# Performance work log

Measured on AMD Instinct MI355X. Metric: run time of the kernel, lower is better.

The kernel has to match this reference:

```python
import jax, jax.numpy as jnp
import numpy as np

B, H, WD, C = 16, 96, 96, 256
WS, SH, NH = 6, 3, 8
N = WS * WS
ALPHA = (2 * 6) ** 0.25  # deepnorm alpha, n_layers=6
SCALE = (C // NH) ** 0.5  # faithful to source: head_dim**0.5 (not **-0.5)
EPS = 1e-5


def _rel_index(ws):
    coords = np.stack(np.meshgrid(np.arange(ws), np.arange(ws), indexing='ij'))  # (2,ws,ws)
    flat = coords.reshape(2, -1)
    rel = (flat[:, :, None] - flat[:, None, :]).transpose(1, 2, 0).copy()
    rel[..., 0] += ws - 1
    rel[..., 1] += ws - 1
    rel[..., 0] *= 2 * ws - 1
    return jnp.asarray(rel.sum(-1))  # (N,N) int


def _attn_mask(h, w, ws, sh):
    img = np.zeros((h, w))
    cnt = 0
    for hs in (slice(0, -ws), slice(-ws, -sh), slice(-sh, None)):
        for wsl in (slice(0, -ws), slice(-ws, -sh), slice(-sh, None)):
            img[hs, wsl] = cnt
            cnt += 1
    win = img.reshape(h // ws, ws, w // ws, ws).transpose(0, 2, 1, 3).reshape(-1, ws * ws)
    diff = win[:, None, :] - win[:, :, None]
    return jnp.asarray(np.where(diff != 0, -100.0, 0.0), jnp.float32)  # (nW,N,N)


def _ln(t, w, b):
    mu = jnp.mean(t, -1, keepdims=True)
    var = jnp.var(t, -1, keepdims=True)
    return (t - mu) * jax.lax.rsqrt(var + EPS) * w + b


def setup_inputs() -> dict:
    key = jax.random.key(0)
    ks = jax.random.split(key, 8)
    d = {
        'x': jax.random.normal(ks[0], (B, H * WD, C), jnp.float32),
        'qkv_w': jax.random.normal(ks[1], (C, 3 * C), jnp.float32) * 0.02,
        'qkv_b': jnp.zeros((3 * C,), jnp.float32),
        'bias_table': jax.random.normal(ks[2], ((2 * WS - 1) ** 2, NH), jnp.float32) * 0.02,
        'proj_w': jax.random.normal(ks[3], (C, C), jnp.float32) * 0.02,
        'proj_b': jnp.zeros((C,), jnp.float32),
        'norm1_w': jnp.ones((C,), jnp.float32),
        'norm1_b': jnp.zeros((C,), jnp.float32),
        'norm2_w': jnp.ones((C,), jnp.float32),
        'norm2_b': jnp.zeros((C,), jnp.float32),
        'fc1_w': jax.random.normal(ks[4], (C, 4 * C), jnp.float32) * 0.02,
        'fc1_b': jnp.zeros((4 * C,), jnp.float32),
        'fc2_w': jax.random.normal(ks[5], (4 * C, C), jnp.float32) * 0.02,
        'fc2_b': jnp.zeros((C,), jnp.float32),
    }
    return d


def reference(x, qkv_w, qkv_b, bias_table, proj_w, proj_b, norm1_w, norm1_b,
              norm2_w, norm2_b, fc1_w, fc1_b, fc2_w, fc2_b):
    hd = C // NH
    nW = (H // WS) * (WD // WS)
    shortcut = x  # (B, L, C), norm_before=False -> post-norm
    xs = x.reshape(B, H, WD, C)
    xs = jnp.roll(xs, (-SH, -SH), axis=(1, 2))  # cyclic shift
    # window partition -> (B*nW, N, C)
    xw = xs.reshape(B, H // WS, WS, WD // WS, WS, C).transpose(0, 1, 3, 2, 4, 5).reshape(B * nW, N, C)
    qkv = (xw @ qkv_w + qkv_b).reshape(B * nW, N, 3, NH, hd).transpose(2, 0, 3, 1, 4)
    q, k, v = qkv[0] * SCALE, qkv[1], qkv[2]
    attn = jnp.einsum('bhnd,bhmd->bhnm', q, k)  # (B*nW, H, N, N)
    bias = bias_table[_rel_index(WS).reshape(-1)].reshape(N, N, NH).transpose(2, 0, 1)
    attn = attn + bias[None]
    mask = _attn_mask(H, WD, WS, SH)  # (nW, N, N)
    attn = attn.reshape(B, nW, NH, N, N) + mask[None, :, None]
    attn = jax.nn.softmax(attn.reshape(B * nW, NH, N, N), axis=-1)
    out = jnp.einsum('bhnm,bhmd->bhnd', attn, v).transpose(0, 2, 1, 3).reshape(B * nW, N, C)
    out = out @ proj_w + proj_b
    # faithful buggy window_reverse: identity permute == plain reshape
    xs = out.reshape(B, H // WS, WS, WD // WS, WS, C).reshape(B, H, WD, C)
    xs = jnp.roll(xs, (SH, SH), axis=(1, 2))
    x1 = _ln(shortcut * ALPHA + xs.reshape(B, H * WD, C), norm1_w, norm1_b)
    hmid = jax.nn.gelu(x1 @ fc1_w + fc1_b, approximate=False)
    x2 = _ln(x1 * ALPHA + (hmid @ fc2_w + fc2_b), norm2_w, norm2_b)
    return x2
```

## Files before the change

kernel.cpp:

```cpp
#include <hip/hip_runtime.h>
#include <math.h>

typedef __bf16 bf16x8 __attribute__((ext_vector_type(8)));
typedef __bf16 bf16x4 __attribute__((ext_vector_type(4)));
typedef short  s16x4  __attribute__((ext_vector_type(4)));
typedef float  f32x4  __attribute__((ext_vector_type(4)));

#define NTOK 147456
#define LTOK 9216
#define ALPHA 1.8612097182041991f
#define QSCALE 5.656854249492380196f
#define MFMA32(a,b,c) __builtin_amdgcn_mfma_f32_16x16x32_bf16((a),(b),(c),0,0,0)
#define SWB(row,kb) ((kb) ^ ((row)&7))

__device__ __forceinline__ f32x4 MFMA16(bf16x4 a, bf16x4 b, f32x4 c) {
#if __has_builtin(__builtin_amdgcn_mfma_f32_16x16x16bf16_1k)
    return __builtin_amdgcn_mfma_f32_16x16x16bf16_1k(*(s16x4*)&a, *(s16x4*)&b, c, 0, 0, 0);
#else
    f32x4 d = c;
    asm volatile("s_nop 1\n\ts_nop 1\n\t"
                 "v_mfma_f32_16x16x16_bf16 %0, %1, %2, %0\n\t"
                 "s_nop 7\n\ts_nop 7"
                 : "+v"(d) : "v"(a), "v"(b));
    return d;
#endif
}

__device__ __forceinline__ float gelu_sig(float x) {
    const float e = __expf(-1.702f * x);
    return x * __builtin_amdgcn_rcpf(1.0f + e);
}

__device__ __forceinline__ void gll16(const void* g, void* l) {
    __builtin_amdgcn_global_load_lds(
        (const __attribute__((address_space(1))) void*)g,
        (__attribute__((address_space(3))) void*)l, 16, 0, 0);
}

__global__ __launch_bounds__(256) void k0_prep(
    const float* __restrict__ qkv_w, const float* __restrict__ proj_w,
    const float* __restrict__ fc1_w, const float* __restrict__ fc2_w,
    __bf16* __restrict__ qkvT, __bf16* __restrict__ projT,
    __bf16* __restrict__ w1T, __bf16* __restrict__ w2T)
{
    const int id = blockIdx.x * 256 + threadIdx.x;
    if (id < 196608) {
        const int o = id >> 8, k = id & 255;
        qkvT[id] = (__bf16)qkv_w[k * 768 + o];
    } else if (id < 262144) {
        const int i = id - 196608, o = i >> 8, k = i & 255;
        projT[i] = (__bf16)proj_w[k * 256 + o];
    } else if (id < 524288) {
        const int i = id - 262144, o = i >> 8, k = i & 255;
        w1T[i] = (__bf16)fc1_w[k * 1024 + o];
    } else {
        const int i = id - 524288, o = i >> 10, k = i & 1023;
        w2T[i] = (__bf16)fc2_w[k * 256 + o];
    }
}

__global__ __launch_bounds__(512, 4) void k1f_qkv_attn(
    const float* __restrict__ x, const __bf16* __restrict__ qkvT,
    const float* __restrict__ qkv_b, const float* __restrict__ bias_table,
    __bf16* __restrict__ attnout)
{
    __shared__ __attribute__((aligned(16))) char SM[77824];
    typedef __bf16 (*a256_t)[256];
    typedef __bf16 (*b32_t)[32];
    a256_t As = (a256_t)SM;
    b32_t  Bs = (b32_t)(SM + 24576);
    int*   srcrow = (int*)(SM + 73728);
    float* bias_s = (float*)(SM + 73920);

    const int t = threadIdx.x;
    const int wid = t >> 6, lane = t & 63;
    const int l15 = lane & 15, lg = lane >> 4;
    const int blk = blockIdx.x;
    const int win = blk & 255;
    const int wh = win >> 4, ww = win & 15;
    const int h = wid;

    if (t < 48) {
        int n = t; if (n > 35) n = 35;
        const int b = blk >> 8;
        const int gh = (wh * 6 + n / 6 + 3) % 96;
        const int gw = (ww * 6 + n % 6 + 3) % 96;
        srcrow[t] = b * LTOK + gh * 96 + gw;
    }
    for (int o = t; o < 968; o += 512) bias_s[o] = bias_table[o];
    __syncthreads();

    for (int o = t; o < 48 * 32; o += 512) {
        const int row = o >> 5, kb = o & 31;
        const float* src = x + (size_t)srcrow[row] * 256 + kb * 8;
        const float4 f0 = *(const float4*)src;
        const float4 f1 = *(const float4*)(src + 4);
        bf16x8 p;
        p[0] = (__bf16)f0.x; p[1] = (__bf16)f0.y; p[2] = (__bf16)f0.z; p[3] = (__bf16)f0.w;
        p[4] = (__bf16)f1.x; p[5] = (__bf16)f1.y; p[6] = (__bf16)f1.z; p[7] = (__bf16)f1.w;
        *(bf16x8*)&As[row][SWB(row, kb) * 8] = p;
    }

    const f32x4 fzero = {0.f, 0.f, 0.f, 0.f};
    f32x4 accQ[2][3], accK[2][3], accV[2][3];
    #pragma unroll
    for (int c = 0; c < 2; ++c)
        #pragma unroll
        for (int r = 0; r < 3; ++r) { accQ[c][r] = fzero; accK[c][r] = fzero; accV[c][r] = fzero; }

    for (int kc = 0; kc < 8; ++kc) {
        __syncthreads();
        #pragma unroll
        for (int i = 0; i < 6; ++i) {
            const int r0 = wid * 96 + i * 16;
            const int row = r0 + (lane >> 2), kbl = lane & 3;
            gll16(qkvT + (size_t)row * 256 + kc * 32 + ((kbl ^ (row & 3)) * 8),
                  &Bs[r0][0]);
        }
        __syncthreads();
        bf16x8 af[3];
        #pragma unroll
        for (int rt = 0; rt < 3; ++rt) {
            const int ar = rt * 16 + l15;
            const int kb = kc * 4 + lg;
            af[rt] = *(const bf16x8*)&As[ar][SWB(ar, kb) * 8];
        }
        #pragma unroll
        for (int ct = 0; ct < 2; ++ct) {
            const int brq = h * 32 + ct * 16 + l15;
            const bf16x8 bq = *(const bf16x8*)&Bs[brq][((lg ^ (brq & 3))) * 8];
            const int brk = 256 + brq;
            const bf16x8 bk = *(const bf16x8*)&Bs[brk][((lg ^ (brk & 3))) * 8];
            const int brv = 512 + brq;
            const bf16x8 bv = *(const bf16x8*)&Bs[brv][((lg ^ (brv & 3))) * 8];
            #pragma unroll
            for (int rt = 0; rt < 3; ++rt) {
                accQ[ct][rt] = MFMA32(bq, af[rt], accQ[ct][rt]);
                accK[ct][rt] = MFMA32(bk, af[rt], accK[ct][rt]);
                accV[ct][rt] = MFMA32(af[rt], bv, accV[ct][rt]);
            }
        }
    }

    bf16x4 qf[3][2], kf[3][2], vf[2][3];
    #pragma unroll
    for (int dh = 0; dh < 2; ++dh) {
        #pragma unroll
        for (int q = 0; q < 4; ++q) {
            const float qb = qkv_b[h * 32 + dh * 16 + lg * 4 + q];
            const float kb = qkv_b[256 + h * 32 + dh * 16 + lg * 4 + q];
            #pragma unroll
            for (int rt = 0; rt < 3; ++rt) {
                qf[rt][dh][q] = (__bf16)((accQ[dh][rt][q] + qb) * QSCALE);
                kf[rt][dh][q] = (__bf16)(accK[dh][rt][q] + kb);
            }
        }
    }
    #pragma unroll
    for (int cd = 0; cd < 2; ++cd) {
        const float vb = qkv_b[512 + h * 32 + cd * 16 + l15];
        #pragma unroll
        for (int c3 = 0; c3 < 3; ++c3)
            #pragma unroll
            for (int q = 0; q < 4; ++q)
                vf[cd][c3][q] = (__bf16)(accV[cd][c3][q] + vb);
    }

    f32x4 s[3][3];
    #pragma unroll
    for (int qt = 0; qt < 3; ++qt)
        #pragma unroll
        for (int c3 = 0; c3 < 3; ++c3) {
            f32x4 acc = MFMA16(kf[c3][0], qf[qt][0], fzero);
            s[qt][c3] = MFMA16(kf[c3][1], qf[qt][1], acc);
        }

    int i2_[3][4], j2_[3][4], g2_[3][4];
    #pragma unroll
    for (int c3 = 0; c3 < 3; ++c3)
        #pragma unroll
        for (int q = 0; q < 4; ++q) {
            const int kt = c3 * 16 + lg * 4 + q;
            const int kk2 = kt < 36 ? kt : 35;
            i2_[c3][q] = kk2 / 6; j2_[c3][q] = kk2 - i2_[c3][q] * 6;
            g2_[c3][q] = ((wh < 15) ? 0 : (i2_[c3][q] < 3 ? 1 : 2)) * 3
                       + ((ww < 15) ? 0 : (j2_[c3][q] < 3 ? 1 : 2));
        }

    bf16x4 pa[3][3];
    #pragma unroll
    for (int qt = 0; qt < 3; ++qt) {
        const int qtok = qt * 16 + l15;
        const int nn = qtok < 36 ? qtok : 35;
        const int i1 = nn / 6, j1 = nn - i1 * 6;
        const int g1 = ((wh < 15) ? 0 : (i1 < 3 ? 1 : 2)) * 3
                     + ((ww < 15) ? 0 : (j1 < 3 ? 1 : 2));
        float vals[3][4];
        float mx = -1e30f;
        #pragma unroll
        for (int c3 = 0; c3 < 3; ++c3)
            #pragma unroll
            for (int q = 0; q < 4; ++q) {
                const int kt = c3 * 16 + lg * 4 + q;
                float v;
                if (kt < 36) {
                    v = s[qt][c3][q]
                      + bias_s[((i1 - i2_[c3][q] + 5) * 11 + (j1 - j2_[c3][q] + 5)) * 8 + h];
                    if (g1 != g2_[c3][q]) v -= 100.0f;
                } else {
                    v = -1e30f;
                }
                vals[c3][q] = v;
                mx = fmaxf(mx, v);
            }
        mx = fmaxf(mx, __shfl_xor(mx, 16));
        mx = fmaxf(mx, __shfl_xor(mx, 32));
        float sum = 0.f;
        #pragma unroll
        for (int c3 = 0; c3 < 3; ++c3)
            #pragma unroll
            for (int q = 0; q < 4; ++q) {
                const float e = __expf(vals[c3][q] - mx);
                vals[c3][q] = e;
                sum += e;
            }
        sum += __shfl_xor(sum, 16);
        sum += __shfl_xor(sum, 32);
        const float inv = 1.0f / sum;
        #pragma unroll
        for (int c3 = 0; c3 < 3; ++c3)
            #pragma unroll
            for (int q = 0; q < 4; ++q)
                pa[qt][c3][q] = (__bf16)(vals[c3][q] * inv);
    }

    const size_t rowbase = (size_t)blk * 36;
    #pragma unroll
    for (int qt = 0; qt < 3; ++qt)
        #pragma unroll
        for (int cd = 0; cd < 2; ++cd) {
            f32x4 o = MFMA16(pa[qt][0], vf[cd][0], fzero);
            o = MFMA16(pa[qt][1], vf[cd][1], o);
            o = MFMA16(pa[qt][2], vf[cd][2], o);
            #pragma unroll
            for (int q = 0; q < 4; ++q) {
                const int n = qt * 16 + lg * 4 + q;
                if (n < 36)
                    attnout[(rowbase + n) * 256 + h * 32 + cd * 16 + l15] = (__bf16)o[q];
            }
        }
}

__global__ __launch_bounds__(512) void k2_proj_ln(
    const __bf16* __restrict__ attnout, const __bf16* __restrict__ projT,
    const float* __restrict__ proj_b, const float* __restrict__ x,
    const float* __restrict__ n1w, const float* __restrict__ n1b,
    __bf16* __restrict__ x1b)
{
    __shared__ __attribute__((aligned(16))) __bf16 As[128][64];
    __shared__ __attribute__((aligned(16))) __bf16 Bs[256][64];
    __shared__ float ps[128][4], ps2[128][4];
    const int t = threadIdx.x;
    const int wid = t >> 6, lane = t & 63;
    const int l15 = lane & 15, lg = lane >> 4;
    const int mb = blockIdx.x;
    const int wm = wid >> 2, wn = wid & 3;

    const f32x4 fzero = {0.f, 0.f, 0.f, 0.f};
    f32x4 acc[4][4];
    #pragma unroll
    for (int i = 0; i < 4; ++i)
        #pragma unroll
        for (int j = 0; j < 4; ++j) acc[i][j] = fzero;

    for (int kc = 0; kc < 4; ++kc) {
        __syncthreads();
        #pragma unroll
        for (int i = 0; i < 2; ++i) {
            const int r0 = wid * 16 + i * 8;
            const int row = r0 + (lane >> 3), kbl = lane & 7;
            gll16(attnout + (size_t)(mb * 128 + row) * 256 + kc * 64 + ((kbl ^ (row & 7)) * 8),
                  &As[r0][0]);
        }
        #pragma unroll
        for (int i = 0; i < 4; ++i) {
            const int r0 = wid * 32 + i * 8;
            const int row = r0 + (lane >> 3), kbl = lane & 7;
            gll16(projT + (size_t)row * 256 + kc * 64 + ((kbl ^ (row & 7)) * 8),
                  &Bs[r0][0]);
        }
        __syncthreads();
        #pragma unroll
        for (int kk = 0; kk < 2; ++kk) {
            bf16x8 af[4], bfr[4];
            #pragma unroll
            for (int rt = 0; rt < 4; ++rt) {
                const int ar = wm * 64 + rt * 16 + l15;
                af[rt] = *(const bf16x8*)&As[ar][((kk * 4 + lg) ^ (ar & 7)) * 8];
            }
            #pragma unroll
            for (int ct = 0; ct < 4; ++ct) {
                const int br = wn * 64 + ct * 16 + l15;
                bfr[ct] = *(const bf16x8*)&Bs[br][((kk * 4 + lg) ^ (br & 7)) * 8];
            }
            #pragma unroll
            for (int rt = 0; rt < 4; ++rt)
                #pragma unroll
                for (int ct = 0; ct < 4; ++ct)
                    acc[rt][ct] = MFMA32(af[rt], bfr[ct], acc[rt][ct]);
        }
    }

    int dtok_[4][4];
    #pragma unroll
    for (int rt = 0; rt < 4; ++rt) {
        #pragma unroll
        for (int q = 0; q < 4; ++q) {
            const int rowl = wm * 64 + rt * 16 + lg * 4 + q;
            const int tok = mb * 128 + rowl;
            const int b = tok / LTOK, l = tok % LTOK;
            const int hh = l / 96, wwp = l % 96;
            const int dtok = b * LTOK + ((hh + 3) % 96) * 96 + ((wwp + 3) % 96);
            dtok_[rt][q] = dtok;
            float s = 0.f, s2 = 0.f;
            #pragma unroll
            for (int ct = 0; ct < 4; ++ct) {
                const int col = wn * 64 + ct * 16 + l15;
                const float v = acc[rt][ct][q] + proj_b[col] + ALPHA * x[(size_t)dtok * 256 + col];
                acc[rt][ct][q] = v;
                s += v; s2 += v * v;
            }
            s  += __shfl_xor(s, 1, 16);  s += __shfl_xor(s, 2, 16);
            s  += __shfl_xor(s, 4, 16);  s += __shfl_xor(s, 8, 16);
            s2 += __shfl_xor(s2, 1, 16); s2 += __shfl_xor(s2, 2, 16);
            s2 += __shfl_xor(s2, 4, 16); s2 += __shfl_xor(s2, 8, 16);
            if (l15 == 0) { ps[rowl][wn] = s; ps2[rowl][wn] = s2; }
        }
    }
    __syncthreads();
    #pragma unroll
    for (int rt = 0; rt < 4; ++rt) {
        #pragma unroll
        for (int q = 0; q < 4; ++q) {
            const int rowl = wm * 64 + rt * 16 + lg * 4 + q;
            const float S  = ps[rowl][0] + ps[rowl][1] + ps[rowl][2] + ps[rowl][3];
            const float S2 = ps2[rowl][0] + ps2[rowl][1] + ps2[rowl][2] + ps2[rowl][3];
            const float mu = S * (1.0f / 256.0f);
            const float var = S2 * (1.0f / 256.0f) - mu * mu;
            const float rstd = rsqrtf(var + 1e-5f);
            __bf16* op = x1b + (size_t)dtok_[rt][q] * 256;
            #pragma unroll
            for (int ct = 0; ct < 4; ++ct) {
                const int col = wn * 64 + ct * 16 + l15;
                op[col] = (__bf16)((acc[rt][ct][q] - mu) * rstd * n1w[col] + n1b[col]);
            }
        }
    }
}

__global__ __launch_bounds__(256, 2) void k3f_mlp(
    const __bf16* __restrict__ x1b, const __bf16* __restrict__ w1T,
    const float* __restrict__ fc1_b, const __bf16* __restrict__ w2T,
    const float* __restrict__ fc2_b, const float* __restrict__ n2w,
    const float* __restrict__ n2b, float* __restrict__ out)
{
    __shared__ __attribute__((aligned(16))) __bf16 w1c[2][32][256];
    __shared__ __attribute__((aligned(16))) __bf16 w2c[2][256][32];
    __shared__ __attribute__((aligned(16))) __bf16 hs[4][32][32];

    const int t = threadIdx.x;
    const int wv = t >> 6, lane = t & 63;
    const int l15 = lane & 15, lg = lane >> 4;
    const int rowbase = blockIdx.x * 128 + wv * 32;

    bf16x8 af[2][8];
    #pragma unroll
    for (int tt = 0; tt < 2; ++tt)
        #pragma unroll
        for (int kk = 0; kk < 8; ++kk)
            af[tt][kk] = *(const bf16x8*)(x1b + (size_t)(rowbase + tt * 16 + l15) * 256 + kk * 32 + lg * 8);

    const f32x4 fzero = {0.f, 0.f, 0.f, 0.f};
    f32x4 acc2[2][16];
    #pragma unroll
    for (int i = 0; i < 2; ++i)
        #pragma unroll
        for (int j = 0; j < 16; ++j) acc2[i][j] = fzero;

    #define STAGE_W(b, c)                                                        \
    {                                                                            \
        _Pragma("unroll")                                                        \
        for (int i = 0; i < 4; ++i) {                                            \
            const int r0 = wv * 8 + i * 2;                                       \
            const int row = r0 + (lane >> 5);                                    \
            const int g = (lane & 31) ^ (row & 7);                               \
            gll16(w1T + (size_t)((c) * 32 + row) * 256 + g * 8, &w1c[b][r0][0]); \
        }                                                                        \
        _Pragma("unroll")                                                        \
        for (int i = 0; i < 4; ++i) {                                            \
            const int r0 = wv * 64 + i * 16;                                     \
            const int row = r0 + (lane >> 2);                                    \
            const int g = (lane & 3) ^ (row & 3);                                \
            gll16(w2T + (size_t)row * 1024 + (c) * 32 + g * 8, &w2c[b][r0][0]);  \
        }                                                                        \
    }

    STAGE_W(0, 0);
    asm volatile("s_waitcnt vmcnt(0)" ::: "memory");
    __builtin_amdgcn_sched_barrier(0);
    __builtin_amdgcn_s_barrier();
    __builtin_amdgcn_sched_barrier(0);

    for (int ch = 0; ch < 32; ++ch) {
        const int cur = ch & 1;
        if (ch < 31) STAGE_W(cur ^ 1, ch + 1);

        f32x4 acc1[2][2];
        #pragma unroll
        for (int i = 0; i < 2; ++i)
            #pragma unroll
            for (int j = 0; j < 2; ++j) acc1[i][j] = fzero;
        #pragma unroll
        for (int kk = 0; kk < 8; ++kk) {
            #pragma unroll
            for (int ht = 0; ht < 2; ++ht) {
                const int hr = ht * 16 + l15;
                const bf16x8 aW = *(const bf16x8*)&w1c[cur][hr][((kk * 4 + lg) ^ (hr & 7)) * 8];
                #pragma unroll
                for (int tt = 0; tt < 2; ++tt)
                    acc1[ht][tt] = MFMA32(aW, af[tt][kk], acc1[ht][tt]);
            }
        }

        #pragma unroll
        for (int ht = 0; ht < 2; ++ht) {
            float bq[4];
            #pragma unroll
            for (int q = 0; q < 4; ++q)
                bq[q] = fc1_b[ch * 32 + ht * 16 + lg * 4 + q];
            #pragma unroll
            for (int tt = 0; tt < 2; ++tt) {
                bf16x4 p;
                #pragma unroll
                for (int q = 0; q < 4; ++q)
                    p[q] = (__bf16)gelu_sig(acc1[ht][tt][q] + bq[q]);
                const int row = tt * 16 + l15;
                const int gW = ht * 2 + (lg >> 1);
                *(bf16x4*)&hs[wv][row][(gW ^ (row & 3)) * 8 + (lg & 1) * 4] = p;
            }
        }

        bf16x8 a2[2];
        #pragma unroll
        for (int tt = 0; tt < 2; ++tt) {
            const int row = tt * 16 + l15;
            a2[tt] = *(const bf16x8*)&hs[wv][row][((lg ^ (row & 3))) * 8];
        }
        #pragma unroll
        for (int ct = 0; ct < 16; ++ct) {
            const int br = ct * 16 + l15;
            const bf16x8 bW = *(const bf16x8*)&w2c[cur][br][((lg ^ (br & 3))) * 8];
            #pragma unroll
            for (int tt = 0; tt < 2; ++tt)
                acc2[tt][ct] = MFMA32(a2[tt], bW, acc2[tt][ct]);
        }

        asm volatile("s_waitcnt vmcnt(0)" ::: "memory");
        __builtin_amdgcn_sched_barrier(0);
        __builtin_amdgcn_s_barrier();
        __builtin_amdgcn_sched_barrier(0);
    }

    #pragma unroll
    for (int tt = 0; tt < 2; ++tt) {
        #pragma unroll
        for (int q = 0; q < 4; ++q) {
            const int grow = tt * 16 + lg * 4 + q;
            const size_t tok = (size_t)(rowbase + grow);
            float s = 0.f, s2 = 0.f;
            float vals[16];
            #pragma unroll
            for (int ct = 0; ct < 16; ++ct) {
                const int col = ct * 16 + l15;
                const float v = acc2[tt][ct][q] + fc2_b[col] + ALPHA * (float)x1b[tok * 256 + col];
                vals[ct] = v;
                s += v; s2 += v * v;
            }
            s  += __shfl_xor(s, 1, 16);  s += __shfl_xor(s, 2, 16);
            s  += __shfl_xor(s, 4, 16);  s += __shfl_xor(s, 8, 16);
            s2 += __shfl_xor(s2, 1, 16); s2 += __shfl_xor(s2, 2, 16);
            s2 += __shfl_xor(s2, 4, 16); s2 += __shfl_xor(s2, 8, 16);
            const float mu = s * (1.0f / 256.0f);
            const float var = s2 * (1.0f / 256.0f) - mu * mu;
            const float rstd = rsqrtf(var + 1e-5f);
            float* op = out + tok * 256;
            #pragma unroll
            for (int ct = 0; ct < 16; ++ct) {
                const int col = ct * 16 + l15;
                op[col] = (vals[ct] - mu) * rstd * n2w[col] + n2b[col];
            }
        }
    }
    #undef STAGE_W
}

extern "C" void kernel_launch(void* const* d_in, const int* in_sizes, int n_in,
                              void* d_out, int out_size, void* d_ws, size_t ws_size,
                              hipStream_t stream)
{
    const float* x          = (const float*)d_in[0];
    const float* qkv_w      = (const float*)d_in[1];
    const float* qkv_b      = (const float*)d_in[2];
    const float* bias_table = (const float*)d_in[3];
    const float* proj_w     = (const float*)d_in[4];
    const float* proj_b     = (const float*)d_in[5];
    const float* n1w        = (const float*)d_in[6];
    const float* n1b        = (const float*)d_in[7];
    const float* n2w        = (const float*)d_in[8];
    const float* n2b        = (const float*)d_in[9];
    const float* fc1_w      = (const float*)d_in[10];
    const float* fc1_b      = (const float*)d_in[11];
    const float* fc2_w      = (const float*)d_in[12];
    const float* fc2_b      = (const float*)d_in[13];
    float* out = (float*)d_out;

    char* ws = (char*)d_ws;
    __bf16* x1b     = (__bf16*)ws;
    __bf16* attnout = (__bf16*)(ws + 75497472);
    __bf16* qkvT    = (__bf16*)(ws + 150994944);
    __bf16* projT   = (__bf16*)(ws + 151388160);
    __bf16* w1T     = (__bf16*)(ws + 151519232);
    __bf16* w2T     = (__bf16*)(ws + 152043520);

    k0_prep<<<3072, 256, 0, stream>>>(qkv_w, proj_w, fc1_w, fc2_w, qkvT, projT, w1T, w2T);
    k1f_qkv_attn<<<4096, 512, 0, stream>>>(x, qkvT, qkv_b, bias_table, attnout);
    k2_proj_ln<<<1152, 512, 0, stream>>>(attnout, projT, proj_b, x, n1w, n1b, x1b);
    k3f_mlp<<<1152, 256, 0, stream>>>(x1b, w1T, fc1_b, w2T, fc2_b, n2w, n2b, out);
}
```

Before: 626.8 us.

## Precompute bias+mask table, load QKV weights directly, stage MLP params in LDS

The prep kernel now builds a combined relative-position-bias and shift-mask table per window type and head, so the attention softmax does a plain vector load instead of computing indices and looking them up per element. The QKV kernel drops the LDS staging of weights and its per-chunk barriers, reading B fragments straight from global/L2 with far less LDS use. The MLP kernel caches biases and norm parameters in LDS, changes the swizzle pattern for w2/hidden tiles, and raises wave priority around the MFMA loops. The direct global weight reads may raise L2 traffic and latency exposure in exchange for higher occupancy and fewer syncs.

```diff
diff --git a/kernel.cpp b/kernel.cpp
--- a/kernel.cpp
+++ b/kernel.cpp
@@ -40,8 +40,10 @@
 __global__ __launch_bounds__(256) void k0_prep(
     const float* __restrict__ qkv_w, const float* __restrict__ proj_w,
     const float* __restrict__ fc1_w, const float* __restrict__ fc2_w,
+    const float* __restrict__ bias_table,
     __bf16* __restrict__ qkvT, __bf16* __restrict__ projT,
-    __bf16* __restrict__ w1T, __bf16* __restrict__ w2T)
+    __bf16* __restrict__ w1T, __bf16* __restrict__ w2T,
+    float* __restrict__ bmask)
 {
     const int id = blockIdx.x * 256 + threadIdx.x;
     if (id < 196608) {
@@ -53,24 +55,36 @@
     } else if (id < 524288) {
         const int i = id - 262144, o = i >> 8, k = i & 255;
         w1T[i] = (__bf16)fc1_w[k * 1024 + o];
-    } else {
+    } else if (id < 786432) {
         const int i = id - 524288, o = i >> 10, k = i & 1023;
         w2T[i] = (__bf16)fc2_w[k * 256 + o];
+    } else if (id < 860160) {
+        const int e = id - 786432;
+        const int m = e % 48;
+        const int n = (e / 48) % 48;
+        const int h = (e / 2304) % 8;
+        const int ty = e / 18432;
+        const int nn = n < 36 ? n : 35, mm = m < 36 ? m : 35;
+        const int i1 = nn / 6, j1 = nn - i1 * 6;
+        const int i2 = mm / 6, j2 = mm - i2 * 6;
+        float v = bias_table[((i1 - i2 + 5) * 11 + (j1 - j2 + 5)) * 8 + h];
+        const int hg1 = (ty & 2) ? (i1 < 3 ? 1 : 2) : 0;
+        const int wg1 = (ty & 1) ? (j1 < 3 ? 1 : 2) : 0;
+        const int hg2 = (ty & 2) ? (i2 < 3 ? 1 : 2) : 0;
+        const int wg2 = (ty & 1) ? (j2 < 3 ? 1 : 2) : 0;
+        if (hg1 * 3 + wg1 != hg2 * 3 + wg2) v -= 100.0f;
+        if (m >= 36) v = -1e30f;
+        bmask[e] = v;
     }
 }
 
 __global__ __launch_bounds__(512, 4) void k1f_qkv_attn(
     const float* __restrict__ x, const __bf16* __restrict__ qkvT,
-    const float* __restrict__ qkv_b, const float* __restrict__ bias_table,
+    const float* __restrict__ qkv_b, const float* __restrict__ bmask,
     __bf16* __restrict__ attnout)
 {
-    __shared__ __attribute__((aligned(16))) char SM[77824];
-    typedef __bf16 (*a256_t)[256];
-    typedef __bf16 (*b32_t)[32];
-    a256_t As = (a256_t)SM;
-    b32_t  Bs = (b32_t)(SM + 24576);
-    int*   srcrow = (int*)(SM + 73728);
-    float* bias_s = (float*)(SM + 73920);
+    __shared__ __attribute__((aligned(16))) __bf16 As[48][256];
+    __shared__ int srcrow[48];
 
     const int t = threadIdx.x;
     const int wid = t >> 6, lane = t & 63;
@@ -87,7 +101,6 @@
         const int gw = (ww * 6 + n % 6 + 3) % 96;
         srcrow[t] = b * LTOK + gh * 96 + gw;
     }
-    for (int o = t; o < 968; o += 512) bias_s[o] = bias_table[o];
     __syncthreads();
 
     for (int o = t; o < 48 * 32; o += 512) {
@@ -100,6 +113,7 @@
         p[4] = (__bf16)f1.x; p[5] = (__bf16)f1.y; p[6] = (__bf16)f1.z; p[7] = (__bf16)f1.w;
         *(bf16x8*)&As[row][SWB(row, kb) * 8] = p;
     }
+    __syncthreads();
 
     const f32x4 fzero = {0.f, 0.f, 0.f, 0.f};
     f32x4 accQ[2][3], accK[2][3], accV[2][3];
@@ -108,31 +122,21 @@
         #pragma unroll
         for (int r = 0; r < 3; ++r) { accQ[c][r] = fzero; accK[c][r] = fzero; accV[c][r] = fzero; }
 
+    const __bf16* bbase = qkvT + (size_t)(h * 32 + l15) * 256 + lg * 8;
+
     for (int kc = 0; kc < 8; ++kc) {
-        __syncthreads();
-        #pragma unroll
-        for (int i = 0; i < 6; ++i) {
-            const int r0 = wid * 96 + i * 16;
-            const int row = r0 + (lane >> 2), kbl = lane & 3;
-            gll16(qkvT + (size_t)row * 256 + kc * 32 + ((kbl ^ (row & 3)) * 8),
-                  &Bs[r0][0]);
-        }
-        __syncthreads();
         bf16x8 af[3];
         #pragma unroll
         for (int rt = 0; rt < 3; ++rt) {
             const int ar = rt * 16 + l15;
-            const int kb = kc * 4 + lg;
-            af[rt] = *(const bf16x8*)&As[ar][SWB(ar, kb) * 8];
+            af[rt] = *(const bf16x8*)&As[ar][SWB(ar, kc * 4 + lg) * 8];
         }
         #pragma unroll
         for (int ct = 0; ct < 2; ++ct) {
-            const int brq = h * 32 + ct * 16 + l15;
-            const bf16x8 bq = *(const bf16x8*)&Bs[brq][((lg ^ (brq & 3))) * 8];
-            const int brk = 256 + brq;
-            const bf16x8 bk = *(const bf16x8*)&Bs[brk][((lg ^ (brk & 3))) * 8];
-            const int brv = 512 + brq;
-            const bf16x8 bv = *(const bf16x8*)&Bs[brv][((lg ^ (brv & 3))) * 8];
+            const __bf16* bp = bbase + (size_t)ct * 16 * 256 + kc * 32;
+            const bf16x8 bq = *(const bf16x8*)bp;
+            const bf16x8 bk = *(const bf16x8*)(bp + 65536);
+            const bf16x8 bv = *(const bf16x8*)(bp + 131072);
             #pragma unroll
             for (int rt = 0; rt < 3; ++rt) {
                 accQ[ct][rt] = MFMA32(bq, af[rt], accQ[ct][rt]);
@@ -142,7 +146,8 @@
         }
     }
 
-    bf16x4 qf[3][2], kf[3][2], vf[2][3];
+    bf16x4 qf[3][2], kf[3][2];
+    bf16x4 vf[2][3];
     #pragma unroll
     for (int dh = 0; dh < 2; ++dh) {
         #pragma unroll
@@ -175,44 +180,27 @@
             s[qt][c3] = MFMA16(kf[c3][1], qf[qt][1], acc);
         }
 
-    int i2_[3][4], j2_[3][4], g2_[3][4];
-    #pragma unroll
-    for (int c3 = 0; c3 < 3; ++c3)
+    const int ty = ((wh == 15) ? 2 : 0) + ((ww == 15) ? 1 : 0);
+    const float* bmp = bmask + (size_t)(ty * 8 + h) * 2304;
+    bf16x4 pa[3][3];
+    #pragma unroll
+    for (int qt = 0; qt < 3; ++qt) {
+        const float* brow = bmp + (qt * 16 + l15) * 48 + lg * 4;
+        const float4 b0 = *(const float4*)brow;
+        const float4 b1 = *(const float4*)(brow + 16);
+        const float4 b2 = *(const float4*)(brow + 32);
+        float vals[3][4];
         #pragma unroll
         for (int q = 0; q < 4; ++q) {
-            const int kt = c3 * 16 + lg * 4 + q;
-            const int kk2 = kt < 36 ? kt : 35;
-            i2_[c3][q] = kk2 / 6; j2_[c3][q] = kk2 - i2_[c3][q] * 6;
-            g2_[c3][q] = ((wh < 15) ? 0 : (i2_[c3][q] < 3 ? 1 : 2)) * 3
-                       + ((ww < 15) ? 0 : (j2_[c3][q] < 3 ? 1 : 2));
-        }
-
-    bf16x4 pa[3][3];
-    #pragma unroll
-    for (int qt = 0; qt < 3; ++qt) {
-        const int qtok = qt * 16 + l15;
-        const int nn = qtok < 36 ? qtok : 35;
-        const int i1 = nn / 6, j1 = nn - i1 * 6;
-        const int g1 = ((wh < 15) ? 0 : (i1 < 3 ? 1 : 2)) * 3
-                     + ((ww < 15) ? 0 : (j1 < 3 ? 1 : 2));
-        float vals[3][4];
+            vals[0][q] = s[qt][0][q] + ((const float*)&b0)[q];
+            vals[1][q] = s[qt][1][q] + ((const float*)&b1)[q];
+            vals[2][q] = s[qt][2][q] + ((const float*)&b2)[q];
+        }
         float mx = -1e30f;
         #pragma unroll
         for (int c3 = 0; c3 < 3; ++c3)
             #pragma unroll
-            for (int q = 0; q < 4; ++q) {
-                const int kt = c3 * 16 + lg * 4 + q;
-                float v;
-                if (kt < 36) {
-                    v = s[qt][c3][q]
-                      + bias_s[((i1 - i2_[c3][q] + 5) * 11 + (j1 - j2_[c3][q] + 5)) * 8 + h];
-                    if (g1 != g2_[c3][q]) v -= 100.0f;
-                } else {
-                    v = -1e30f;
-                }
-                vals[c3][q] = v;
-                mx = fmaxf(mx, v);
-            }
+            for (int q = 0; q < 4; ++q) mx = fmaxf(mx, vals[c3][q]);
         mx = fmaxf(mx, __shfl_xor(mx, 16));
         mx = fmaxf(mx, __shfl_xor(mx, 32));
         float sum = 0.f;
@@ -367,11 +355,15 @@
     __shared__ __attribute__((aligned(16))) __bf16 w1c[2][32][256];
     __shared__ __attribute__((aligned(16))) __bf16 w2c[2][256][32];
     __shared__ __attribute__((aligned(16))) __bf16 hs[4][32][32];
+    __shared__ float fc1b_s[1024], fc2b_s[256], n2w_s[256], n2b_s[256];
 
     const int t = threadIdx.x;
     const int wv = t >> 6, lane = t & 63;
     const int l15 = lane & 15, lg = lane >> 4;
     const int rowbase = blockIdx.x * 128 + wv * 32;
+
+    for (int o = t; o < 1024; o += 256) fc1b_s[o] = fc1_b[o];
+    if (t < 256) { fc2b_s[t] = fc2_b[t]; n2w_s[t] = n2w[t]; n2b_s[t] = n2b[t]; }
 
     bf16x8 af[2][8];
     #pragma unroll
@@ -400,7 +392,7 @@
         for (int i = 0; i < 4; ++i) {                                            \
             const int r0 = wv * 64 + i * 16;                                     \
             const int row = r0 + (lane >> 2);                                    \
-            const int g = (lane & 3) ^ (row & 3);                                \
+            const int g = (lane & 3) ^ ((row >> 1) & 3);                         \
             gll16(w2T + (size_t)row * 1024 + (c) * 32 + g * 8, &w2c[b][r0][0]);  \
         }                                                                        \
     }
@@ -420,6 +412,7 @@
         for (int i = 0; i < 2; ++i)
             #pragma unroll
             for (int j = 0; j < 2; ++j) acc1[i][j] = fzero;
+        __builtin_amdgcn_s_setprio(1);
         #pragma unroll
         for (int kk = 0; kk < 8; ++kk) {
             #pragma unroll
@@ -431,13 +424,14 @@
                     acc1[ht][tt] = MFMA32(aW, af[tt][kk], acc1[ht][tt]);
             }
         }
+        __builtin_amdgcn_s_setprio(0);
 
         #pragma unroll
         for (int ht = 0; ht < 2; ++ht) {
             float bq[4];
             #pragma unroll
             for (int q = 0; q < 4; ++q)
-                bq[q] = fc1_b[ch * 32 + ht * 16 + lg * 4 + q];
+                bq[q] = fc1b_s[ch * 32 + ht * 16 + lg * 4 + q];
             #pragma unroll
             for (int tt = 0; tt < 2; ++tt) {
                 bf16x4 p;
@@ -446,7 +440,7 @@
                     p[q] = (__bf16)gelu_sig(acc1[ht][tt][q] + bq[q]);
                 const int row = tt * 16 + l15;
                 const int gW = ht * 2 + (lg >> 1);
-                *(bf16x4*)&hs[wv][row][(gW ^ (row & 3)) * 8 + (lg & 1) * 4] = p;
+                *(bf16x4*)&hs[wv][row][(gW ^ ((row >> 1) & 3)) * 8 + (lg & 1) * 4] = p;
             }
         }
 
@@ -454,16 +448,18 @@
         #pragma unroll
         for (int tt = 0; tt < 2; ++tt) {
             const int row = tt * 16 + l15;
-            a2[tt] = *(const bf16x8*)&hs[wv][row][((lg ^ (row & 3))) * 8];
-        }
+            a2[tt] = *(const bf16x8*)&hs[wv][row][((lg ^ ((row >> 1) & 3))) * 8];
+        }
+        __builtin_amdgcn_s_setprio(1);
         #pragma unroll
         for (int ct = 0; ct < 16; ++ct) {
             const int br = ct * 16 + l15;
-            const bf16x8 bW = *(const bf16x8*)&w2c[cur][br][((lg ^ (br & 3))) * 8];
+            const bf16x8 bW = *(const bf16x8*)&w2c[cur][br][((lg ^ ((br >> 1) & 3))) * 8];
             #pragma unroll
             for (int tt = 0; tt < 2; ++tt)
                 acc2[tt][ct] = MFMA32(a2[tt], bW, acc2[tt][ct]);
         }
+        __builtin_amdgcn_s_setprio(0);
 
         asm volatile("s_waitcnt vmcnt(0)" ::: "memory");
         __builtin_amdgcn_sched_barrier(0);
@@ -482,7 +478,7 @@
             #pragma unroll
             for (int ct = 0; ct < 16; ++ct) {
                 const int col = ct * 16 + l15;
-                const float v = acc2[tt][ct][q] + fc2_b[col] + ALPHA * (float)x1b[tok * 256 + col];
+                const float v = acc2[tt][ct][q] + fc2b_s[col] + ALPHA * (float)x1b[tok * 256 + col];
                 vals[ct] = v;
                 s += v; s2 += v * v;
             }
@@ -497,7 +493,7 @@
             #pragma unroll
             for (int ct = 0; ct < 16; ++ct) {
                 const int col = ct * 16 + l15;
-                op[col] = (vals[ct] - mu) * rstd * n2w[col] + n2b[col];
+                op[col] = (vals[ct] - mu) * rstd * n2w_s[col] + n2b_s[col];
             }
         }
     }
@@ -531,9 +527,11 @@
     __bf16* projT   = (__bf16*)(ws + 151388160);
     __bf16* w1T     = (__bf16*)(ws + 151519232);
     __bf16* w2T     = (__bf16*)(ws + 152043520);
-
-    k0_prep<<<3072, 256, 0, stream>>>(qkv_w, proj_w, fc1_w, fc2_w, qkvT, projT, w1T, w2T);
-    k1f_qkv_attn<<<4096, 512, 0, stream>>>(x, qkvT, qkv_b, bias_table, attnout);
+    float*  bmask   = (float*)(ws + 152567808);
+
+    k0_prep<<<3360, 256, 0, stream>>>(qkv_w, proj_w, fc1_w, fc2_w, bias_table,
+                                      qkvT, projT, w1T, w2T, bmask);
+    k1f_qkv_attn<<<4096, 512, 0, stream>>>(x, qkvT, qkv_b, bmask, attnout);
     k2_proj_ln<<<1152, 512, 0, stream>>>(attnout, projT, proj_b, x, n1w, n1b, x1b);
     k3f_mlp<<<1152, 256, 0, stream>>>(x1b, w1T, fc1_b, w2T, fc2_b, n2w, n2b, out);
 }
```

Result: faster. 597.4 us, median of 3 (-4.7%).
